# Performance work log

Measured on AMD Instinct MI355X. Metric: run time of the kernel, lower is better.

## Reference

```python
import jax, jax.numpy as jnp
import numpy as np

N = 8192       # nodes
IN_F = 512     # in_features
OUT_F = 256    # out_features


def setup_inputs() -> dict:
    key = jax.random.key(0)
    k1, k2, k3, k4 = jax.random.split(key, 4)
    # xavier_uniform-like scales for params
    w_scale = 1.414 * (6.0 / (IN_F + OUT_F)) ** 0.5
    a_scale = 1.414 * (6.0 / (2 * OUT_F + 1)) ** 0.5
    x = jax.random.normal(k1, (N, IN_F), jnp.float32)
    W = jax.random.uniform(k2, (IN_F, OUT_F), jnp.float32, -w_scale, w_scale)
    a = jax.random.uniform(k3, (2 * OUT_F, 1), jnp.float32, -a_scale, a_scale)
    adj = jax.random.randint(k4, (N, N), 0, 2, jnp.int32)
    return {"x": x, "W": W, "a": a, "adj": adj}


def reference(x, W, a, adj):
    # h = x @ W : [N, OUT_F]
    h = x @ W
    f = W.shape[1]
    a1, a2 = a[:f], a[f:]          # each [OUT_F, 1]
    # Original builds a_input[i,j] = concat(h_i, h_j) then matmuls with a.
    # Equivalent decomposition: e[i,j] = h_i . a1 + h_j . a2
    e = (h @ a1) + (h @ a2).T      # [N, N]
    neg = jnp.float32(-9e15)
    attention = jnp.where(adj > 0, e, neg)   # no softmax in the original
    h_prime = attention @ h        # [N, OUT_F]
    return h_prime
```

## Files before the change

kernel.cpp:

```cpp
#include <hip/hip_runtime.h>


#define NEG_BIG (-9000000000000000.0f)
#define POS_BIG (9000000000000000.0f)

typedef __bf16 bf16x8 __attribute__((ext_vector_type(8)));
typedef float f32x16 __attribute__((ext_vector_type(16)));

static __device__ __forceinline__ unsigned short f2bf(float f) {
  unsigned u = __builtin_bit_cast(unsigned, f);
  u = u + 0x7FFFu + ((u >> 16) & 1u);
  return (unsigned short)(u >> 16);
}
static __device__ __forceinline__ float bfbits2f(unsigned hi16) {
  return __builtin_bit_cast(float, hi16 << 16);
}
static __device__ __forceinline__ unsigned pk2(float a, float b) {
  return (unsigned)f2bf(a) | ((unsigned)f2bf(b) << 16);
}
static __device__ __forceinline__ unsigned m2(int a, int b) {
  return (unsigned)(a + (b << 16)) * 0x3F80u;
}
static __device__ __forceinline__ bf16x8 asbf(int4 q) {
  return __builtin_bit_cast(bf16x8, q);
}
static __device__ __forceinline__ f32x16 mfma(bf16x8 a, int4 b, f32x16 c) {
  return __builtin_amdgcn_mfma_f32_32x32x16_bf16(a, asbf(b), c, 0, 0, 0);
}

__global__ void k1a_wt(const float* __restrict__ W, unsigned short* __restrict__ WT,
                       float* __restrict__ T) {
  const int i = blockIdx.x * 256 + threadIdx.x;
  const int k = i >> 8, n = i & 255;
  WT[n * 512 + k] = f2bf(W[i]);
  if (blockIdx.x == 0) T[threadIdx.x] = 0.f;
}

__global__ __launch_bounds__(256) void k1b_h(const float* __restrict__ x,
    const unsigned short* __restrict__ WT, unsigned short* __restrict__ hP) {
  __shared__ unsigned short XS[64 * 264];
  const int t = threadIdx.x;
  const int mt = blockIdx.x;
  const int m0 = mt << 5;
  const int row = t >> 3, c7 = t & 7;
  const float* xr = x + (size_t)(m0 + row) * 512 + c7 * 4;
  const int gb = c7 >> 1, off = (t & 1) * 4;
#pragma unroll
  for (int j = 0; j < 16; ++j) {
    float4 v = *(const float4*)(xr + 32 * j);
    *(uint2*)&XS[(gb + 4 * j) * 264 + row * 8 + off] =
        make_uint2(pk2(v.x, v.y), pk2(v.z, v.w));
  }
  __syncthreads();
  const int w = t >> 6, l = t & 63, l31 = l & 31, lh = l >> 5;
  f32x16 acc0, acc1;
  for (int i = 0; i < 16; ++i) { acc0[i] = 0.f; acc1[i] = 0.f; }
  const int nt0 = w * 2;
  const unsigned short* w0 = WT + (size_t)(nt0 * 32 + l31) * 512 + lh * 8;
  const unsigned short* w1 = w0 + 32 * 512;
  const char* XB = (const char*)XS + lh * 528 + l31 * 16;
#pragma unroll 4
  for (int ks = 0; ks < 32; ++ks) {
    bf16x8 Af = *(const bf16x8*)(XB + ks * 1056);
    int4 b0 = *(const int4*)(w0 + ks * 16);
    int4 b1 = *(const int4*)(w1 + ks * 16);
    acc0 = mfma(Af, b0, acc0);
    acc1 = mfma(Af, b1, acc1);
  }
#pragma unroll
  for (int reg = 0; reg < 16; ++reg) {
    const int mm = (reg & 3) + 8 * (reg >> 2) + 4 * lh;
    hP[(size_t)mt * 8192 + (nt0 * 32 + l31) * 32 + mm] = f2bf(acc0[reg]);
    hP[(size_t)mt * 8192 + ((nt0 + 1) * 32 + l31) * 32 + mm] = f2bf(acc1[reg]);
  }
}

__global__ __launch_bounds__(256) void k2_colsum(const unsigned short* __restrict__ hP,
                                                 float* __restrict__ T) {
  const int t = threadIdx.x;
  const int b = blockIdx.x;
  const int4* p = (const int4*)(hP + (size_t)b * 8192 + t * 32);
  int4 q0 = p[0], q1 = p[1], q2 = p[2], q3 = p[3];
  float s = 0.f;
  const unsigned* u0 = (const unsigned*)&q0;
  const unsigned* u1 = (const unsigned*)&q1;
  const unsigned* u2 = (const unsigned*)&q2;
  const unsigned* u3 = (const unsigned*)&q3;
#pragma unroll
  for (int i = 0; i < 4; ++i) {
    s += bfbits2f(u0[i] & 0xFFFFu) + bfbits2f(u0[i] >> 16);
    s += bfbits2f(u1[i] & 0xFFFFu) + bfbits2f(u1[i] >> 16);
    s += bfbits2f(u2[i] & 0xFFFFu) + bfbits2f(u2[i] >> 16);
    s += bfbits2f(u3[i] & 0xFFFFu) + bfbits2f(u3[i] >> 16);
  }
  atomicAdd(&T[t], s);
}

__global__ void k2b_init(const float* __restrict__ T, float* __restrict__ out) {
  const int i = blockIdx.x * 256 + threadIdx.x;
  const int n4 = (i & 63) * 4;
  float4 tv = *(const float4*)(T + n4);
  float4 o;
  o.x = NEG_BIG * tv.x; o.y = NEG_BIG * tv.y;
  o.z = NEG_BIG * tv.z; o.w = NEG_BIG * tv.w;
  ((float4*)out)[i] = o;
}

template<int MODE>
__global__ __launch_bounds__(256, 2) void k3_att(const int* __restrict__ adj,
    const unsigned short* __restrict__ hP, float* __restrict__ outp) {
  __shared__ unsigned short S[4][2][8 * 264];
  const int t = threadIdx.x, blk = blockIdx.x;
  const int s = blk & 7;
  const int rg = blk >> 3;
  const int w = t >> 6, l = t & 63, l31 = l & 31, lh = l >> 5;
  const int rtile = rg * 2 + (w >> 1);
  const int nh = w & 1;
  const int sr = l >> 4, j4 = (l & 15) << 2;
  const int* aB = adj + (size_t)(rtile * 32 + sr) * 8192 + s * 1024 + j4;
  unsigned short* const Sw0 = &S[w][0][0];
  unsigned short* const Sw1 = &S[w][1][0];
  const int woff = (j4 >> 3) * 264 + sr * 8 + (j4 & 7);

  const unsigned short* hB = hP + (size_t)(s * 32) * 8192
                              + (size_t)(nh * 128 + l31) * 32 + lh * 8;

  f32x16 acc[4];
#pragma unroll
  for (int nt = 0; nt < 4; ++nt)
#pragma unroll
    for (int i = 0; i < 16; ++i) acc[nt][i] = 0.f;

  int4 gA[8], gB[8], Bv[16];

#define ALOAD(dst, it)                                                      \
  _Pragma("unroll")                                                         \
  for (int q = 0; q < 8; ++q)                                               \
    dst[q] = *(const int4*)(aB + (size_t)q * 4 * 8192 + (it) * 64);
#define APACK(buf, src)                                                     \
  _Pragma("unroll")                                                         \
  for (int q = 0; q < 8; ++q)                                               \
    *(uint2*)&buf[woff + q * 32] =                                          \
        make_uint2(m2(src[q].x, src[q].y), m2(src[q].z, src[q].w));
#define BLOAD(it)                                                           \
  {                                                                         \
    const unsigned short* hb = hB + (size_t)(it) * 2 * 8192;                \
    _Pragma("unroll")                                                       \
    for (int pb = 0; pb < 2; ++pb)                                          \
      _Pragma("unroll")                                                     \
      for (int kh = 0; kh < 2; ++kh)                                        \
        _Pragma("unroll")                                                   \
        for (int nt = 0; nt < 4; ++nt)                                      \
          Bv[(pb * 2 + kh) * 4 + nt] =                                      \
              *(const int4*)(hb + pb * 8192 + nt * 1024 + kh * 16);         \
  }
#define COMP(buf)                                                           \
  {                                                                         \
    const char* Ab = (const char*)(buf) + lh * 528 + l31 * 16;              \
    _Pragma("unroll")                                                       \
    for (int ks = 0; ks < 4; ++ks) {                                        \
      bf16x8 Af = *(const bf16x8*)(Ab + ks * 1056);                         \
      _Pragma("unroll")                                                     \
      for (int nt = 0; nt < 4; ++nt)                                        \
        acc[nt] = mfma(Af, Bv[ks * 4 + nt], acc[nt]);                       \
    }                                                                       \
  }

  ALOAD(gA, 0)
  ALOAD(gB, 1)
  APACK(Sw0, gA)

#pragma unroll 1
  for (int r = 0; r < 16; r += 2) {
    BLOAD(r)
    if (r + 2 < 16) { ALOAD(gA, r + 2) }
    APACK(Sw1, gB)
    COMP(Sw0)
    BLOAD(r + 1)
    if (r + 3 < 16) { ALOAD(gB, r + 3) }
    if (r + 2 < 16) { APACK(Sw0, gA) }
    COMP(Sw1)
  }
#undef ALOAD
#undef APACK
#undef BLOAD
#undef COMP

#pragma unroll
  for (int nt = 0; nt < 4; ++nt) {
    const int nn = nh * 128 + nt * 32 + l31;
#pragma unroll
    for (int reg = 0; reg < 16; ++reg) {
      const int rr = rtile * 32 + (reg & 3) + 8 * (reg >> 2) + 4 * lh;
      if (MODE == 0) {
        outp[(size_t)s * 2097152 + (size_t)rr * 256 + nn] = acc[nt][reg];
      } else {
        atomicAdd(outp + (size_t)rr * 256 + nn, POS_BIG * acc[nt][reg]);
      }
    }
  }
}

__global__ __launch_bounds__(256) void k4_reduce(const float* __restrict__ P,
    const float* __restrict__ T, float* __restrict__ out) {
  const int i = blockIdx.x * 256 + threadIdx.x;
  float4 tv = *(const float4*)(T + (i & 63) * 4);
  const float4* P4 = (const float4*)P;
  float sx = 0.f, sy = 0.f, sz = 0.f, sw = 0.f;
#pragma unroll
  for (int sp = 0; sp < 8; ++sp) {
    float4 v = P4[(size_t)sp * 524288 + i];
    sx += v.x; sy += v.y; sz += v.z; sw += v.w;
  }
  float4 o;
  o.x = POS_BIG * sx + NEG_BIG * tv.x;
  o.y = POS_BIG * sy + NEG_BIG * tv.y;
  o.z = POS_BIG * sz + NEG_BIG * tv.z;
  o.w = POS_BIG * sw + NEG_BIG * tv.w;
  ((float4*)out)[i] = o;
}

extern "C" void kernel_launch(void* const* d_in, const int* in_sizes, int n_in,
                              void* d_out, int out_size, void* d_ws, size_t ws_size,
                              hipStream_t stream) {
  const float* x = (const float*)d_in[0];
  const float* W = (const float*)d_in[1];
  const int* adj = (const int*)d_in[3];
  float* out = (float*)d_out;
  char* ws = (char*)d_ws;
  unsigned short* WT = (unsigned short*)(ws);
  unsigned short* hP = (unsigned short*)(ws + (1 << 20));
  float* T = (float*)(ws + (6 << 20));
  float* P = (float*)(ws + (8 << 20));

  const bool fit = ws_size >= ((size_t)(8 << 20) + (size_t)64 * 1024 * 1024);

  k1a_wt<<<512, 256, 0, stream>>>(W, WT, T);
  k1b_h<<<256, 256, 0, stream>>>(x, WT, hP);
  k2_colsum<<<256, 256, 0, stream>>>(hP, T);
  if (fit) {
    k3_att<0><<<1024, 256, 0, stream>>>(adj, hP, P);
    k4_reduce<<<2048, 256, 0, stream>>>(P, T, out);
  } else {
    k2b_init<<<2048, 256, 0, stream>>>(T, out);
    k3_att<1><<<1024, 256, 0, stream>>>(adj, hP, out);
  }
}
```

Measured before the change: 473.0 us.

## Double per-wave row tile in attention kernel to reuse h fragments

```diff
diff --git a/kernel.cpp b/kernel.cpp
--- a/kernel.cpp
+++ b/kernel.cpp
@@ -109,77 +109,77 @@
 template<int MODE>
 __global__ __launch_bounds__(256, 2) void k3_att(const int* __restrict__ adj,
     const unsigned short* __restrict__ hP, float* __restrict__ outp) {
-  __shared__ unsigned short S[4][2][8 * 264];
+  __shared__ unsigned short S[4][2][4 * 512];
   const int t = threadIdx.x, blk = blockIdx.x;
   const int s = blk & 7;
   const int rg = blk >> 3;
   const int w = t >> 6, l = t & 63, l31 = l & 31, lh = l >> 5;
-  const int rtile = rg * 2 + (w >> 1);
+  const int rt = rg * 2 + (w >> 1);
   const int nh = w & 1;
-  const int sr = l >> 4, j4 = (l & 15) << 2;
-  const int* aB = adj + (size_t)(rtile * 32 + sr) * 8192 + s * 1024 + j4;
+
+  const int* aB = adj + (size_t)(rt * 64 + (l >> 3)) * 8192 + s * 1024 + (l & 7) * 4;
+  const int woff = ((l & 7) >> 1) * 512 + (l >> 3) * 8 + (l & 1) * 4;
   unsigned short* const Sw0 = &S[w][0][0];
   unsigned short* const Sw1 = &S[w][1][0];
-  const int woff = (j4 >> 3) * 264 + sr * 8 + (j4 & 7);
-
   const unsigned short* hB = hP + (size_t)(s * 32) * 8192
                               + (size_t)(nh * 128 + l31) * 32 + lh * 8;
-
-  f32x16 acc[4];
-#pragma unroll
-  for (int nt = 0; nt < 4; ++nt)
-#pragma unroll
-    for (int i = 0; i < 16; ++i) acc[nt][i] = 0.f;
-
-  int4 gA[8], gB[8], Bv[16];
-
-#define ALOAD(dst, it)                                                      \
+  const int fr = lh * 1024 + l31 * 16;
+
+  f32x16 acc[2][4];
+#pragma unroll
+  for (int mt = 0; mt < 2; ++mt)
+#pragma unroll
+    for (int nt = 0; nt < 4; ++nt)
+#pragma unroll
+      for (int i = 0; i < 16; ++i) acc[mt][nt][i] = 0.f;
+
+  int4 gA[8], Bv[8];
+
+#define ALOAD(it)                                                           \
   _Pragma("unroll")                                                         \
   for (int q = 0; q < 8; ++q)                                               \
-    dst[q] = *(const int4*)(aB + (size_t)q * 4 * 8192 + (it) * 64);
-#define APACK(buf, src)                                                     \
+    gA[q] = *(const int4*)(aB + (size_t)q * 8 * 8192 + (it) * 32);
+#define APACK(buf)                                                          \
   _Pragma("unroll")                                                         \
   for (int q = 0; q < 8; ++q)                                               \
-    *(uint2*)&buf[woff + q * 32] =                                          \
-        make_uint2(m2(src[q].x, src[q].y), m2(src[q].z, src[q].w));
+    *(uint2*)&buf[woff + q * 64] =                                          \
+        make_uint2(m2(gA[q].x, gA[q].y), m2(gA[q].z, gA[q].w));
 #define BLOAD(it)                                                           \
   {                                                                         \
-    const unsigned short* hb = hB + (size_t)(it) * 2 * 8192;                \
+    const unsigned short* hb = hB + (size_t)(it) * 8192;                    \
     _Pragma("unroll")                                                       \
-    for (int pb = 0; pb < 2; ++pb)                                          \
+    for (int ks = 0; ks < 2; ++ks)                                          \
       _Pragma("unroll")                                                     \
-      for (int kh = 0; kh < 2; ++kh)                                        \
-        _Pragma("unroll")                                                   \
-        for (int nt = 0; nt < 4; ++nt)                                      \
-          Bv[(pb * 2 + kh) * 4 + nt] =                                      \
-              *(const int4*)(hb + pb * 8192 + nt * 1024 + kh * 16);         \
+      for (int nt = 0; nt < 4; ++nt)                                        \
+        Bv[ks * 4 + nt] = *(const int4*)(hb + nt * 1024 + ks * 16);         \
   }
 #define COMP(buf)                                                           \
   {                                                                         \
-    const char* Ab = (const char*)(buf) + lh * 528 + l31 * 16;              \
+    const char* Ab = (const char*)(buf) + fr;                               \
     _Pragma("unroll")                                                       \
-    for (int ks = 0; ks < 4; ++ks) {                                        \
-      bf16x8 Af = *(const bf16x8*)(Ab + ks * 1056);                         \
+    for (int ks = 0; ks < 2; ++ks) {                                        \
+      bf16x8 A0 = *(const bf16x8*)(Ab + ks * 2048);                         \
+      bf16x8 A1 = *(const bf16x8*)(Ab + ks * 2048 + 512);                   \
       _Pragma("unroll")                                                     \
-      for (int nt = 0; nt < 4; ++nt)                                        \
-        acc[nt] = mfma(Af, Bv[ks * 4 + nt], acc[nt]);                       \
+      for (int nt = 0; nt < 4; ++nt) {                                      \
+        acc[0][nt] = mfma(A0, Bv[ks * 4 + nt], acc[0][nt]);                 \
+        acc[1][nt] = mfma(A1, Bv[ks * 4 + nt], acc[1][nt]);                 \
+      }                                                                     \
     }                                                                       \
   }
 
-  ALOAD(gA, 0)
-  ALOAD(gB, 1)
-  APACK(Sw0, gA)
+  ALOAD(0)
+  APACK(Sw0)
+  ALOAD(1)
 
 #pragma unroll 1
-  for (int r = 0; r < 16; r += 2) {
-    BLOAD(r)
-    if (r + 2 < 16) { ALOAD(gA, r + 2) }
-    APACK(Sw1, gB)
-    COMP(Sw0)
-    BLOAD(r + 1)
-    if (r + 3 < 16) { ALOAD(gB, r + 3) }
-    if (r + 2 < 16) { APACK(Sw0, gA) }
-    COMP(Sw1)
+  for (int it = 0; it < 32; ++it) {
+    unsigned short* const Scur = (it & 1) ? Sw1 : Sw0;
+    unsigned short* const Snxt = (it & 1) ? Sw0 : Sw1;
+    BLOAD(it)
+    if (it + 1 < 32) { APACK(Snxt) }
+    if (it + 2 < 32) { ALOAD(it + 2) }
+    COMP(Scur)
   }
 #undef ALOAD
 #undef APACK
@@ -187,18 +187,20 @@
 #undef COMP
 
 #pragma unroll
-  for (int nt = 0; nt < 4; ++nt) {
-    const int nn = nh * 128 + nt * 32 + l31;
-#pragma unroll
-    for (int reg = 0; reg < 16; ++reg) {
-      const int rr = rtile * 32 + (reg & 3) + 8 * (reg >> 2) + 4 * lh;
-      if (MODE == 0) {
-        outp[(size_t)s * 2097152 + (size_t)rr * 256 + nn] = acc[nt][reg];
-      } else {
-        atomicAdd(outp + (size_t)rr * 256 + nn, POS_BIG * acc[nt][reg]);
+  for (int mt = 0; mt < 2; ++mt)
+#pragma unroll
+    for (int nt = 0; nt < 4; ++nt) {
+      const int nn = nh * 128 + nt * 32 + l31;
+#pragma unroll
+      for (int reg = 0; reg < 16; ++reg) {
+        const int rr = rt * 64 + mt * 32 + (reg & 3) + 8 * (reg >> 2) + 4 * lh;
+        if (MODE == 0) {
+          outp[(size_t)s * 2097152 + (size_t)rr * 256 + nn] = acc[mt][nt][reg];
+        } else {
+          atomicAdd(outp + (size_t)rr * 256 + nn, POS_BIG * acc[mt][nt][reg]);
+        }
       }
     }
-  }
 }
 
 __global__ __launch_bounds__(256) void k4_reduce(const float* __restrict__ P,
@@ -239,10 +241,10 @@
   k1b_h<<<256, 256, 0, stream>>>(x, WT, hP);
   k2_colsum<<<256, 256, 0, stream>>>(hP, T);
   if (fit) {
-    k3_att<0><<<1024, 256, 0, stream>>>(adj, hP, P);
+    k3_att<0><<<512, 256, 0, stream>>>(adj, hP, P);
     k4_reduce<<<2048, 256, 0, stream>>>(P, T, out);
   } else {
     k2b_init<<<2048, 256, 0, stream>>>(T, out);
-    k3_att<1><<<1024, 256, 0, stream>>>(adj, hP, out);
-  }
-}
+    k3_att<1><<<512, 256, 0, stream>>>(adj, hP, out);
+  }
+}
```

New measurement: 461.3 us. 2.5% less time.
